# Kernel optimization log

Hardware: AMD Instinct MI355X
Metric: run time of the kernel (lower is better)

Reference implementation:

```python
import jax, jax.numpy as jnp
import numpy as np

N_NODES = 50000


def gcn_conv(x, src, dst, W, b):
    # PyG GCNConv: h = x @ W; symmetric norm with added self-loops; out = A_hat h + b
    h = x @ W
    deg = jax.ops.segment_sum(jnp.ones_like(src, dtype=h.dtype), dst,
                              num_segments=N_NODES) + 1.0  # +1 self-loop
    dis = jax.lax.rsqrt(deg)  # deg >= 1, safe
    msg = h[src] * (dis[src] * dis[dst])[:, None]          # [E,H] gather + scale
    agg = jax.ops.segment_sum(msg, dst, num_segments=N_NODES)
    agg = agg + h * (dis * dis)[:, None]                   # self-loop contribution
    return agg + b


def link_pred(zs, e, Wp, bp):
    # zs: [L,N,H]; gather endpoints along node dim, per-edge cross-layer Gram matrix
    s = zs[:, e[0]]                                # [L,E,H]
    d = zs[:, e[1]]                                # [L,E,H]
    dot = jnp.einsum('leh,meh->elm', s, d)         # [E,L,L] per-edge bmm
    emb = dot.reshape(dot.shape[0], -1)            # [E,L*L]
    return emb @ Wp + bp                           # [E,1] logits (activation=False)


def reference(x, ei, pos, neg, W0, b0, Wh, bh, Wp, bp):
    src, dst = ei[0], ei[1]
    h = jax.nn.relu(gcn_conv(x, src, dst, W0, b0))
    embs = [h]
    for i in range(Wh.shape[0]):  # fixed small layer count
        h = jax.nn.relu(gcn_conv(h, src, dst, Wh[i], bh[i]))
        embs.append(h)
    zs = jnp.stack(embs, axis=0)                   # [L,N,H]
    pos_pred = link_pred(zs, pos, Wp, bp)
    neg_pred = link_pred(zs, neg, Wp, bp)
    logits = jnp.concatenate([pos_pred, neg_pred], axis=0)  # [2E,1]
    # faithful to source: targets all zero except row index == n_pos set to 1
    targets = jnp.zeros_like(logits).at[pos_pred.shape[0]].set(1.0)
    # BCEWithLogitsLoss (mean, numerically stable)
    loss = jnp.mean(jnp.clip(logits, 0.0) - logits * targets
                    + jnp.log1p(jnp.exp(-jnp.abs(logits))))
    return loss


def setup_inputs():
    key = jax.random.key(0)
    ks = jax.random.split(key, 10)
    N, E, EP, IN, H, L = 50000, 800000, 100000, 128, 64, 4
    x = jax.random.normal(ks[0], (N, IN), jnp.float32)
    ei = jax.random.randint(ks[1], (2, E), 0, N, dtype=jnp.int32)
    pos = jax.random.randint(ks[2], (2, EP), 0, N, dtype=jnp.int32)
    neg = jax.random.randint(ks[3], (2, EP), 0, N, dtype=jnp.int32)
    def u(k, shape, fan_in):
        s = 1.0 / np.sqrt(fan_in)
        return jax.random.uniform(k, shape, jnp.float32, -s, s)
    W0 = u(ks[4], (IN, H), IN)
    b0 = u(ks[5], (H,), IN)
    Wh = u(ks[6], (L - 1, H, H), H)
    bh = u(ks[7], (L - 1, H), H)
    Wp = u(ks[8], (L * L, 1), L * L)
    bp = u(ks[9], (1,), L * L)
    return {"x": x, "ei": ei, "pos": pos, "neg": neg, "W0": W0, "b0": b0,
            "Wh": Wh, "bh": bh, "Wp": Wp, "bp": bp}
```

## Files before the change

kernel.cpp:

```cpp
#include <hip/hip_runtime.h>
#include <hip/hip_bf16.h>
#include <math.h>

constexpr int N_NODES = 50000;
constexpr int HD = 64;
constexpr int NBKT = (N_NODES + 255) / 256;

typedef float floatx2 __attribute__((ext_vector_type(2)));

__device__ __forceinline__ float bf2f(unsigned short u) {
    return __uint_as_float((unsigned)u << 16);
}
__device__ __forceinline__ unsigned short f2bf(float f) {
    __hip_bfloat16 b = __float2bfloat16(f);
    return *(unsigned short*)&b;
}
__device__ __forceinline__ unsigned pack_fp8x4(float a, float b, float c, float d) {
    unsigned p = __builtin_amdgcn_cvt_pk_fp8_f32(a, b, 0u, false);
    return __builtin_amdgcn_cvt_pk_fp8_f32(c, d, p, true);
}
__device__ __forceinline__ float dot16_fp8(uint4 u, uint4 d) {
    const unsigned uu[4] = {u.x, u.y, u.z, u.w};
    const unsigned dd[4] = {d.x, d.y, d.z, d.w};
    float s = 0.f;
#pragma unroll
    for (int q = 0; q < 4; ++q) {
        floatx2 ua = __builtin_amdgcn_cvt_pk_f32_fp8(uu[q], false);
        floatx2 ub = __builtin_amdgcn_cvt_pk_f32_fp8(uu[q], true);
        floatx2 da = __builtin_amdgcn_cvt_pk_f32_fp8(dd[q], false);
        floatx2 db = __builtin_amdgcn_cvt_pk_f32_fp8(dd[q], true);
        s = fmaf(ua[0], da[0], s);
        s = fmaf(ua[1], da[1], s);
        s = fmaf(ub[0], db[0], s);
        s = fmaf(ub[1], db[1], s);
    }
    return s;
}

__global__ __launch_bounds__(256) void bhist_kernel(const int* __restrict__ dst,
                                                    int* __restrict__ bcnt, int E) {
    __shared__ int lh[256];
    const int t = threadIdx.x;
    lh[t] = 0;
    __syncthreads();
    const int beg = blockIdx.x * 2048;
    const int end = min(beg + 2048, E);
    for (int i = beg + t; i < end; i += 256)
        atomicAdd(&lh[dst[i] >> 8], 1);
    __syncthreads();
    if (t < NBKT && lh[t]) atomicAdd(&bcnt[t], lh[t]);
}

__global__ __launch_bounds__(256) void bscan_kernel(const int* __restrict__ bcnt,
                                                    int* __restrict__ bbase,
                                                    int* __restrict__ gcur) {
    const int t = threadIdx.x;
    const int v = (t < NBKT) ? bcnt[t] : 0;
    const int lane = t & 63, wid = t >> 6;
    int incl = v;
#pragma unroll
    for (int o = 1; o <= 32; o <<= 1) {
        int u = __shfl_up(incl, o);
        if (lane >= o) incl += u;
    }
    __shared__ int wt[4];
    if (lane == 63) wt[wid] = incl;
    __syncthreads();
    int base = 0;
    for (int w = 0; w < wid; ++w) base += wt[w];
    const int excl = base + incl - v;
    if (t < NBKT) { bbase[t] = excl; gcur[t] = excl; }
    if (t == NBKT - 1) bbase[NBKT] = excl + v;
}

__global__ __launch_bounds__(256) void partition_kernel(const int* __restrict__ src,
                                                        const int* __restrict__ dst,
                                                        int* __restrict__ gcur,
                                                        unsigned* __restrict__ pk, int E) {
    __shared__ unsigned epk[8192];
    __shared__ int lh[NBKT], lbase[NBKT], lcur[NBKT];
    const int t = threadIdx.x;
    for (int i = t; i < NBKT; i += 256) { lh[i] = 0; lcur[i] = 0; }
    __syncthreads();
    const int beg = blockIdx.x * 8192;
    const int end = min(beg + 8192, E);
    for (int i = beg + t; i < end; i += 256) {
        const int s = src[i], d = dst[i];
        const int bkt = d >> 8;
        epk[i - beg] = ((unsigned)bkt << 24) | ((unsigned)(d & 255) << 16) | (unsigned)s;
        atomicAdd(&lh[bkt], 1);
    }
    __syncthreads();
    for (int i = t; i < NBKT; i += 256)
        if (lh[i]) lbase[i] = atomicAdd(&gcur[i], lh[i]);
    __syncthreads();
    for (int i = beg + t; i < end; i += 256) {
        const unsigned p = epk[i - beg];
        const int bkt = p >> 24;
        const int r = atomicAdd(&lcur[bkt], 1);
        pk[lbase[bkt] + r] = p;
    }
}

__global__ __launch_bounds__(256) void bsort_kernel(const unsigned* __restrict__ pk,
                                                    const int* __restrict__ bbase,
                                                    int* __restrict__ off,
                                                    float* __restrict__ dis,
                                                    int* __restrict__ csr, int E, int N) {
    __shared__ int ncnt[256], nbs[256], ncur[256];
    __shared__ int wt[4];
    const int t = threadIdx.x;
    const int bkt = blockIdx.x;
    const int gb = bbase[bkt], ge = bbase[bkt + 1];
    ncnt[t] = 0; ncur[t] = 0;
    __syncthreads();
    for (int i = gb + t; i < ge; i += 256)
        atomicAdd(&ncnt[(pk[i] >> 16) & 255], 1);
    __syncthreads();
    const int v = ncnt[t];
    const int lane = t & 63, wid = t >> 6;
    int incl = v;
#pragma unroll
    for (int o = 1; o <= 32; o <<= 1) {
        int u = __shfl_up(incl, o);
        if (lane >= o) incl += u;
    }
    if (lane == 63) wt[wid] = incl;
    __syncthreads();
    int base = 0;
    for (int w = 0; w < wid; ++w) base += wt[w];
    nbs[t] = base + incl - v;
    const int n = bkt * 256 + t;
    if (n < N) {
        off[n] = gb + nbs[t];
        dis[n] = rsqrtf((float)v + 1.0f);
        if (n == N - 1) off[N] = E;
    }
    __syncthreads();
    for (int i = gb + t; i < ge; i += 256) {
        const unsigned p = pk[i];
        const int dl = (p >> 16) & 255;
        const int r = atomicAdd(&ncur[dl], 1);
        csr[gb + nbs[dl] + r] = (int)(p & 0xFFFFu);
    }
}

template <int K, bool INBF16>
__global__ __launch_bounds__(256) void gemm_kernel(const void* __restrict__ in_,
                                                   const float* __restrict__ W,
                                                   unsigned short* __restrict__ out16,
                                                   unsigned* __restrict__ out8, int N) {
    __shared__ float xs[64][68];
    __shared__ float Wl[64][64];
    const int t = threadIdx.x;
    const int row0 = blockIdx.x * 64;
    const int cq = t & 15, rq = t >> 4;
    float acc[4][4] = {{0.f}};
    for (int kc = 0; kc < K; kc += 64) {
#pragma unroll
        for (int it = 0; it < 4; ++it) {
            const int idx = it * 256 + t;
            const int r = idx >> 4, c4 = idx & 15;
            const int rr = min(row0 + r, N - 1);
            if constexpr (INBF16) {
                const unsigned short* in16 = (const unsigned short*)in_;
                const ushort4 v = *(const ushort4*)(in16 + (size_t)rr * K + kc + c4 * 4);
                *(float4*)(&xs[r][c4 * 4]) = make_float4(bf2f(v.x), bf2f(v.y), bf2f(v.z), bf2f(v.w));
            } else {
                const float* inf = (const float*)in_;
                *(float4*)(&xs[r][c4 * 4]) = *(const float4*)(inf + (size_t)rr * K + kc + c4 * 4);
            }
            *(float4*)(&Wl[r][c4 * 4]) = *(const float4*)(W + (size_t)(kc + r) * HD + c4 * 4);
        }
        __syncthreads();
#pragma unroll
        for (int k4 = 0; k4 < 16; ++k4) {
            float a[4][4], b[4][4];
#pragma unroll
            for (int i = 0; i < 4; ++i)
                *(float4*)a[i] = *(const float4*)(&xs[rq * 4 + i][k4 * 4]);
#pragma unroll
            for (int kk = 0; kk < 4; ++kk)
                *(float4*)b[kk] = *(const float4*)(&Wl[k4 * 4 + kk][cq * 4]);
#pragma unroll
            for (int kk = 0; kk < 4; ++kk)
#pragma unroll
                for (int i = 0; i < 4; ++i)
#pragma unroll
                    for (int j = 0; j < 4; ++j)
                        acc[i][j] = fmaf(a[i][kk], b[kk][j], acc[i][j]);
        }
        __syncthreads();
    }
#pragma unroll
    for (int i = 0; i < 4; ++i) {
        const int r = row0 + rq * 4 + i;
        if (r < N) {
            ushort4 o;
            o.x = f2bf(acc[i][0]); o.y = f2bf(acc[i][1]);
            o.z = f2bf(acc[i][2]); o.w = f2bf(acc[i][3]);
            *(ushort4*)(out16 + (size_t)r * HD + cq * 4) = o;
            out8[(size_t)r * 16 + cq] = pack_fp8x4(acc[i][0], acc[i][1], acc[i][2], acc[i][3]);
        }
    }
}

__global__ __launch_bounds__(256) void agg_kernel(const int* __restrict__ csr,
                                                  const int* __restrict__ off,
                                                  const float* __restrict__ dis,
                                                  const unsigned short* __restrict__ h16,
                                                  const unsigned* __restrict__ h8,
                                                  const float* __restrict__ b,
                                                  unsigned short* __restrict__ z16, int N) {
    const int lane = threadIdx.x & 63;
    const int wid  = threadIdx.x >> 6;
    const int n = blockIdx.x * 4 + wid;
    if (n >= N) return;
    const int beg = off[n];
    const int c = min(off[n + 1] - beg, 64);
    int   s_l = 0;
    float w_l = 0.f;
    if (lane < c) {
        s_l = csr[beg + lane];
        w_l = dis[s_l];
    }
    const float dn = dis[n];
    const int g = lane >> 3;
    const int p = lane & 7;
    float a[8];
#pragma unroll
    for (int j = 0; j < 8; ++j) a[j] = 0.f;
    int   sE = __shfl(s_l, g);
    float wE = __shfl(w_l, g);
    uint2 hv = *(const uint2*)(h8 + (size_t)sE * 16 + p * 2);
    for (int e = 8; e < c; e += 8) {
        const int   sN = __shfl(s_l, e + g);
        const float wN = __shfl(w_l, e + g);
        const uint2 nv = *(const uint2*)(h8 + (size_t)sN * 16 + p * 2);
        floatx2 f01 = __builtin_amdgcn_cvt_pk_f32_fp8(hv.x, false);
        floatx2 f23 = __builtin_amdgcn_cvt_pk_f32_fp8(hv.x, true);
        floatx2 f45 = __builtin_amdgcn_cvt_pk_f32_fp8(hv.y, false);
        floatx2 f67 = __builtin_amdgcn_cvt_pk_f32_fp8(hv.y, true);
        a[0] = fmaf(f01[0], wE, a[0]); a[1] = fmaf(f01[1], wE, a[1]);
        a[2] = fmaf(f23[0], wE, a[2]); a[3] = fmaf(f23[1], wE, a[3]);
        a[4] = fmaf(f45[0], wE, a[4]); a[5] = fmaf(f45[1], wE, a[5]);
        a[6] = fmaf(f67[0], wE, a[6]); a[7] = fmaf(f67[1], wE, a[7]);
        hv = nv; wE = wN;
    }
    {
        floatx2 f01 = __builtin_amdgcn_cvt_pk_f32_fp8(hv.x, false);
        floatx2 f23 = __builtin_amdgcn_cvt_pk_f32_fp8(hv.x, true);
        floatx2 f45 = __builtin_amdgcn_cvt_pk_f32_fp8(hv.y, false);
        floatx2 f67 = __builtin_amdgcn_cvt_pk_f32_fp8(hv.y, true);
        a[0] = fmaf(f01[0], wE, a[0]); a[1] = fmaf(f01[1], wE, a[1]);
        a[2] = fmaf(f23[0], wE, a[2]); a[3] = fmaf(f23[1], wE, a[3]);
        a[4] = fmaf(f45[0], wE, a[4]); a[5] = fmaf(f45[1], wE, a[5]);
        a[6] = fmaf(f67[0], wE, a[6]); a[7] = fmaf(f67[1], wE, a[7]);
    }
#pragma unroll
    for (int st = 8; st <= 32; st <<= 1)
#pragma unroll
        for (int j = 0; j < 8; ++j) a[j] += __shfl_xor(a[j], st);
    if (g == 0) {
        const uint4 sv = *(const uint4*)(h16 + (size_t)n * HD + p * 8);
        const unsigned ss[4] = {sv.x, sv.y, sv.z, sv.w};
        const float4 b0 = *(const float4*)(b + p * 8);
        const float4 b1 = *(const float4*)(b + p * 8 + 4);
        const float bb[8] = {b0.x, b0.y, b0.z, b0.w, b1.x, b1.y, b1.z, b1.w};
        float o[8];
#pragma unroll
        for (int q = 0; q < 4; ++q) {
            o[2 * q]     = a[2 * q]     + __uint_as_float(ss[q] << 16) * dn;
            o[2 * q + 1] = a[2 * q + 1] + __uint_as_float(ss[q] & 0xFFFF0000u) * dn;
        }
#pragma unroll
        for (int j = 0; j < 8; ++j) o[j] = fmaxf(fmaf(o[j], dn, bb[j]), 0.f);
        ushort4 o0, o1;
        o0.x = f2bf(o[0]); o0.y = f2bf(o[1]); o0.z = f2bf(o[2]); o0.w = f2bf(o[3]);
        o1.x = f2bf(o[4]); o1.y = f2bf(o[5]); o1.z = f2bf(o[6]); o1.w = f2bf(o[7]);
        unsigned short* zp = z16 + (size_t)n * HD + p * 8;
        *(ushort4*)zp = o0;
        *(ushort4*)(zp + 4) = o1;
    }
}

__global__ __launch_bounds__(256) void uprep_kernel(const unsigned short* __restrict__ z16,
                                                    const float* __restrict__ Wp,
                                                    unsigned* __restrict__ u8,
                                                    unsigned* __restrict__ d8, int N) {
    const int i = blockIdx.x * blockDim.x + threadIdx.x;
    const int total = N * HD;
    if (i >= total) return;
    const size_t NH = (size_t)N_NODES * HD;
    const float z0 = bf2f(z16[0 * NH + i]), z1 = bf2f(z16[1 * NH + i]);
    const float z2 = bf2f(z16[2 * NH + i]), z3 = bf2f(z16[3 * NH + i]);
    d8[i] = pack_fp8x4(z0, z1, z2, z3);
    const float u0 = z0 * Wp[0] + z1 * Wp[4] + z2 * Wp[8]  + z3 * Wp[12];
    const float u1 = z0 * Wp[1] + z1 * Wp[5] + z2 * Wp[9]  + z3 * Wp[13];
    const float u2 = z0 * Wp[2] + z1 * Wp[6] + z2 * Wp[10] + z3 * Wp[14];
    const float u3 = z0 * Wp[3] + z1 * Wp[7] + z2 * Wp[11] + z3 * Wp[15];
    u8[i] = pack_fp8x4(u0, u1, u2, u3);
}

__global__ __launch_bounds__(256) void linkpred_kernel(const unsigned* __restrict__ u8,
                                                       const unsigned* __restrict__ d8,
                                                       const int* __restrict__ pos,
                                                       const int* __restrict__ neg,
                                                       const float* __restrict__ bp,
                                                       double* __restrict__ acc, int EP) {
    const int lane = threadIdx.x & 63;
    const int wid  = threadIdx.x >> 6;
    const int grp  = lane >> 4;
    const int p    = lane & 15;
    const float bpv = bp[0];
    int gw = blockIdx.x * 4 + wid;
    const int nw = gridDim.x * 4;
    const int nchunks = (2 * EP) >> 3;
    float lsum = 0.f;
    for (int c0 = gw; c0 < nchunks; c0 += nw) {
        const int c = __builtin_amdgcn_readfirstlane(c0);
        const int i0 = c << 3;
        const bool is_pos = i0 < EP;
        const int* __restrict__ eptr = is_pos ? pos : neg;
        const int jj0 = is_pos ? i0 : i0 - EP;
        int idx = 0;
        if (lane < 16)
            idx = (lane < 8) ? eptr[jj0 + lane] : eptr[EP + jj0 + lane - 8];
        const int e0a = __shfl(idx, grp),     e1a = __shfl(idx, 8 + grp);
        const int e0b = __shfl(idx, 4 + grp), e1b = __shfl(idx, 12 + grp);
        const uint4 ua = *(const uint4*)(u8 + (size_t)e0a * HD + p * 4);
        const uint4 da = *(const uint4*)(d8 + (size_t)e1a * HD + p * 4);
        const uint4 ub = *(const uint4*)(u8 + (size_t)e0b * HD + p * 4);
        const uint4 db = *(const uint4*)(d8 + (size_t)e1b * HD + p * 4);
        float tA = dot16_fp8(ua, da);
        float tB = dot16_fp8(ub, db);
#pragma unroll
        for (int st = 1; st <= 8; st <<= 1) {
            tA += __shfl_xor(tA, st);
            tB += __shfl_xor(tB, st);
        }
        const float ga = __shfl(tA, (lane & 3) * 16);
        const float gb = __shfl(tB, (lane & 3) * 16);
        const float tt = (lane < 4) ? ga : gb;
        if (lane < 8) {
            float logit  = tt + bpv;
            float target = (i0 + lane == EP) ? 1.f : 0.f;
            lsum += fmaxf(logit, 0.f) - logit * target + log1pf(expf(-fabsf(logit)));
        }
    }
#pragma unroll
    for (int o = 32; o >= 1; o >>= 1) lsum += __shfl_xor(lsum, o);
    __shared__ float wsum[4];
    if (lane == 0) wsum[wid] = lsum;
    __syncthreads();
    if (threadIdx.x == 0) {
        double bs = (double)wsum[0] + (double)wsum[1] + (double)wsum[2] + (double)wsum[3];
        atomicAdd(acc, bs);
    }
}

__global__ void loss_final(const double* __restrict__ acc, float* __restrict__ out, int denom) {
    out[0] = (float)(acc[0] / (double)denom);
}

extern "C" void kernel_launch(void* const* d_in, const int* in_sizes, int n_in,
                              void* d_out, int out_size, void* d_ws, size_t ws_size,
                              hipStream_t stream) {
    const float* x   = (const float*)d_in[0];
    const int*   ei  = (const int*)d_in[1];
    const int*   pos = (const int*)d_in[2];
    const int*   neg = (const int*)d_in[3];
    const float* W0  = (const float*)d_in[4];
    const float* b0  = (const float*)d_in[5];
    const float* Wh  = (const float*)d_in[6];
    const float* bh  = (const float*)d_in[7];
    const float* Wp  = (const float*)d_in[8];
    const float* bp  = (const float*)d_in[9];
    const int E  = in_sizes[1] / 2;
    const int EP = in_sizes[2] / 2;
    const int N  = N_NODES;
    const size_t NH = (size_t)N * HD;

    char* ws = (char*)d_ws;
    size_t off_b = 0;
    auto alloc = [&](size_t bytes) { char* p = ws + off_b; off_b = (off_b + bytes + 255) & ~(size_t)255; return p; };
    unsigned short* h16 = (unsigned short*)alloc(NH * sizeof(unsigned short));
    unsigned*       h8  = (unsigned*)alloc(NH);
    unsigned short* z16 = (unsigned short*)alloc(4 * NH * sizeof(unsigned short));
    unsigned*       u8  = (unsigned*)alloc(NH * sizeof(unsigned));
    unsigned*       d8  = (unsigned*)alloc(NH * sizeof(unsigned));
    float* dis = (float*)alloc((size_t)N * sizeof(float));
    int*   off = (int*)alloc((size_t)(N + 1) * sizeof(int));
    int*   csr = (int*)alloc((size_t)E * sizeof(int));
    unsigned* pk = (unsigned*)alloc((size_t)E * sizeof(unsigned));
    int*   bbase = (int*)alloc((size_t)(NBKT + 1) * sizeof(int));
    int*   gcur  = (int*)alloc((size_t)NBKT * sizeof(int));
    char*  zbase = ws + off_b;
    int*   bcnt = (int*)alloc((size_t)NBKT * sizeof(int));
    double* acc = (double*)alloc(sizeof(double));
    size_t zero_bytes = (size_t)((char*)acc - zbase) + sizeof(double);

    hipMemsetAsync(zbase, 0, zero_bytes, stream);

    const int* src = ei;
    const int* dst = ei + E;

    bhist_kernel<<<(E + 2047) / 2048, 256, 0, stream>>>(dst, bcnt, E);
    bscan_kernel<<<1, 256, 0, stream>>>(bcnt, bbase, gcur);
    partition_kernel<<<(E + 8191) / 8192, 256, 0, stream>>>(src, dst, gcur, pk, E);
    bsort_kernel<<<NBKT, 256, 0, stream>>>(pk, bbase, off, dis, csr, E, N);

    const int agg_blocks  = (N + 3) / 4;
    const int gemm_blocks = (N + 63) / 64;

    gemm_kernel<128, false><<<gemm_blocks, 256, 0, stream>>>(x, W0, h16, h8, N);
    agg_kernel<<<agg_blocks, 256, 0, stream>>>(csr, off, dis, h16, h8, b0, z16, N);

    for (int l = 1; l < 4; ++l) {
        unsigned short* zprev = z16 + (size_t)(l - 1) * NH;
        unsigned short* zcur  = z16 + (size_t)l * NH;
        gemm_kernel<64, true><<<gemm_blocks, 256, 0, stream>>>(zprev, Wh + (size_t)(l - 1) * HD * HD, h16, h8, N);
        agg_kernel<<<agg_blocks, 256, 0, stream>>>(csr, off, dis, h16, h8,
                                                   bh + (size_t)(l - 1) * HD, zcur, N);
    }

    uprep_kernel<<<(N * HD + 255) / 256, 256, 0, stream>>>(z16, Wp, u8, d8, N);
    linkpred_kernel<<<2048, 256, 0, stream>>>(u8, d8, pos, neg, bp, acc, EP);
    loss_final<<<1, 1, 0, stream>>>(acc, (float*)d_out, 2 * EP);
}
```

Baseline: 276.7 us.

## Fuse first GEMM with histogram, uprep into final aggregation, loss finalize into linkpred

Folds the degree-bucket histogram into the first GEMM launch as extra blocks, so the two independent jobs share one grid. The separate uprep pass moves into the last aggregation kernel, which builds the fp8 u/d tensors from the fresh layer output and the earlier layers it already has in hand. The final loss division moves into linkpred through an atomic ticket on the last block. The goal is fewer kernel launches and one fewer full pass over z16, at the cost of a heavier final aggregation kernel and a ticket-based completion check.

```diff
diff --git a/kernel.cpp b/kernel.cpp
--- a/kernel.cpp
+++ b/kernel.cpp
@@ -37,18 +37,70 @@
     return s;
 }
 
-__global__ __launch_bounds__(256) void bhist_kernel(const int* __restrict__ dst,
-                                                    int* __restrict__ bcnt, int E) {
-    __shared__ int lh[256];
+__global__ __launch_bounds__(256) void gemm128_bhist_kernel(
+        const float* __restrict__ in_, const float* __restrict__ W,
+        unsigned short* __restrict__ out16, unsigned* __restrict__ out8,
+        const int* __restrict__ dst, int* __restrict__ bcnt,
+        int N, int E, int nGemm) {
+    __shared__ float xs[64][68];
+    __shared__ float Wl[64][64];
     const int t = threadIdx.x;
-    lh[t] = 0;
-    __syncthreads();
-    const int beg = blockIdx.x * 2048;
-    const int end = min(beg + 2048, E);
-    for (int i = beg + t; i < end; i += 256)
-        atomicAdd(&lh[dst[i] >> 8], 1);
-    __syncthreads();
-    if (t < NBKT && lh[t]) atomicAdd(&bcnt[t], lh[t]);
+    if ((int)blockIdx.x >= nGemm) {
+        int* lh = (int*)&xs[0][0];
+        lh[t] = 0;
+        __syncthreads();
+        const int beg = ((int)blockIdx.x - nGemm) * 2048;
+        const int end = min(beg + 2048, E);
+        for (int i = beg + t; i < end; i += 256)
+            atomicAdd(&lh[dst[i] >> 8], 1);
+        __syncthreads();
+        if (t < NBKT && lh[t]) atomicAdd(&bcnt[t], lh[t]);
+        return;
+    }
+    constexpr int K = 128;
+    const int row0 = blockIdx.x * 64;
+    const int cq = t & 15, rq = t >> 4;
+    float acc[4][4] = {{0.f}};
+    for (int kc = 0; kc < K; kc += 64) {
+#pragma unroll
+        for (int it = 0; it < 4; ++it) {
+            const int idx = it * 256 + t;
+            const int r = idx >> 4, c4 = idx & 15;
+            const int rr = min(row0 + r, N - 1);
+            *(float4*)(&xs[r][c4 * 4]) = *(const float4*)(in_ + (size_t)rr * K + kc + c4 * 4);
+            *(float4*)(&Wl[r][c4 * 4]) = *(const float4*)(W + (size_t)(kc + r) * HD + c4 * 4);
+        }
+        __syncthreads();
+#pragma unroll
+        for (int k4 = 0; k4 < 16; ++k4) {
+            float a[4][4], b[4][4];
+#pragma unroll
+            for (int i = 0; i < 4; ++i)
+                *(float4*)a[i] = *(const float4*)(&xs[rq * 4 + i][k4 * 4]);
+#pragma unroll
+            for (int kk = 0; kk < 4; ++kk)
+                *(float4*)b[kk] = *(const float4*)(&Wl[k4 * 4 + kk][cq * 4]);
+#pragma unroll
+            for (int kk = 0; kk < 4; ++kk)
+#pragma unroll
+                for (int i = 0; i < 4; ++i)
+#pragma unroll
+                    for (int j = 0; j < 4; ++j)
+                        acc[i][j] = fmaf(a[i][kk], b[kk][j], acc[i][j]);
+        }
+        __syncthreads();
+    }
+#pragma unroll
+    for (int i = 0; i < 4; ++i) {
+        const int r = row0 + rq * 4 + i;
+        if (r < N) {
+            ushort4 o;
+            o.x = f2bf(acc[i][0]); o.y = f2bf(acc[i][1]);
+            o.z = f2bf(acc[i][2]); o.w = f2bf(acc[i][3]);
+            *(ushort4*)(out16 + (size_t)r * HD + cq * 4) = o;
+            out8[(size_t)r * 16 + cq] = pack_fp8x4(acc[i][0], acc[i][1], acc[i][2], acc[i][3]);
+        }
+    }
 }
 
 __global__ __launch_bounds__(256) void bscan_kernel(const int* __restrict__ bcnt,
@@ -145,32 +197,26 @@
     }
 }
 
-template <int K, bool INBF16>
-__global__ __launch_bounds__(256) void gemm_kernel(const void* __restrict__ in_,
-                                                   const float* __restrict__ W,
-                                                   unsigned short* __restrict__ out16,
-                                                   unsigned* __restrict__ out8, int N) {
+__global__ __launch_bounds__(256) void gemm64_kernel(const unsigned short* __restrict__ in16,
+                                                     const float* __restrict__ W,
+                                                     unsigned short* __restrict__ out16,
+                                                     unsigned* __restrict__ out8, int N) {
+    constexpr int K = 64;
     __shared__ float xs[64][68];
     __shared__ float Wl[64][64];
     const int t = threadIdx.x;
     const int row0 = blockIdx.x * 64;
     const int cq = t & 15, rq = t >> 4;
     float acc[4][4] = {{0.f}};
-    for (int kc = 0; kc < K; kc += 64) {
+    {
 #pragma unroll
         for (int it = 0; it < 4; ++it) {
             const int idx = it * 256 + t;
             const int r = idx >> 4, c4 = idx & 15;
             const int rr = min(row0 + r, N - 1);
-            if constexpr (INBF16) {
-                const unsigned short* in16 = (const unsigned short*)in_;
-                const ushort4 v = *(const ushort4*)(in16 + (size_t)rr * K + kc + c4 * 4);
-                *(float4*)(&xs[r][c4 * 4]) = make_float4(bf2f(v.x), bf2f(v.y), bf2f(v.z), bf2f(v.w));
-            } else {
-                const float* inf = (const float*)in_;
-                *(float4*)(&xs[r][c4 * 4]) = *(const float4*)(inf + (size_t)rr * K + kc + c4 * 4);
-            }
-            *(float4*)(&Wl[r][c4 * 4]) = *(const float4*)(W + (size_t)(kc + r) * HD + c4 * 4);
+            const ushort4 v = *(const ushort4*)(in16 + (size_t)rr * K + c4 * 4);
+            *(float4*)(&xs[r][c4 * 4]) = make_float4(bf2f(v.x), bf2f(v.y), bf2f(v.z), bf2f(v.w));
+            *(float4*)(&Wl[r][c4 * 4]) = *(const float4*)(W + (size_t)r * HD + c4 * 4);
         }
         __syncthreads();
 #pragma unroll
@@ -190,7 +236,6 @@
                     for (int j = 0; j < 4; ++j)
                         acc[i][j] = fmaf(a[i][kk], b[kk][j], acc[i][j]);
         }
-        __syncthreads();
     }
 #pragma unroll
     for (int i = 0; i < 4; ++i) {
@@ -205,13 +250,18 @@
     }
 }
 
+template <bool FINAL>
 __global__ __launch_bounds__(256) void agg_kernel(const int* __restrict__ csr,
                                                   const int* __restrict__ off,
                                                   const float* __restrict__ dis,
                                                   const unsigned short* __restrict__ h16,
                                                   const unsigned* __restrict__ h8,
                                                   const float* __restrict__ b,
-                                                  unsigned short* __restrict__ z16, int N) {
+                                                  unsigned short* __restrict__ z16out,
+                                                  const unsigned short* __restrict__ zall,
+                                                  const float* __restrict__ Wp,
+                                                  unsigned* __restrict__ u8,
+                                                  unsigned* __restrict__ d8, int N) {
     const int lane = threadIdx.x & 63;
     const int wid  = threadIdx.x >> 6;
     const int n = blockIdx.x * 4 + wid;
@@ -273,33 +323,45 @@
             o[2 * q]     = a[2 * q]     + __uint_as_float(ss[q] << 16) * dn;
             o[2 * q + 1] = a[2 * q + 1] + __uint_as_float(ss[q] & 0xFFFF0000u) * dn;
         }
-#pragma unroll
-        for (int j = 0; j < 8; ++j) o[j] = fmaxf(fmaf(o[j], dn, bb[j]), 0.f);
-        ushort4 o0, o1;
-        o0.x = f2bf(o[0]); o0.y = f2bf(o[1]); o0.z = f2bf(o[2]); o0.w = f2bf(o[3]);
-        o1.x = f2bf(o[4]); o1.y = f2bf(o[5]); o1.z = f2bf(o[6]); o1.w = f2bf(o[7]);
-        unsigned short* zp = z16 + (size_t)n * HD + p * 8;
-        *(ushort4*)zp = o0;
-        *(ushort4*)(zp + 4) = o1;
-    }
-}
-
-__global__ __launch_bounds__(256) void uprep_kernel(const unsigned short* __restrict__ z16,
-                                                    const float* __restrict__ Wp,
-                                                    unsigned* __restrict__ u8,
-                                                    unsigned* __restrict__ d8, int N) {
-    const int i = blockIdx.x * blockDim.x + threadIdx.x;
-    const int total = N * HD;
-    if (i >= total) return;
-    const size_t NH = (size_t)N_NODES * HD;
-    const float z0 = bf2f(z16[0 * NH + i]), z1 = bf2f(z16[1 * NH + i]);
-    const float z2 = bf2f(z16[2 * NH + i]), z3 = bf2f(z16[3 * NH + i]);
-    d8[i] = pack_fp8x4(z0, z1, z2, z3);
-    const float u0 = z0 * Wp[0] + z1 * Wp[4] + z2 * Wp[8]  + z3 * Wp[12];
-    const float u1 = z0 * Wp[1] + z1 * Wp[5] + z2 * Wp[9]  + z3 * Wp[13];
-    const float u2 = z0 * Wp[2] + z1 * Wp[6] + z2 * Wp[10] + z3 * Wp[14];
-    const float u3 = z0 * Wp[3] + z1 * Wp[7] + z2 * Wp[11] + z3 * Wp[15];
-    u8[i] = pack_fp8x4(u0, u1, u2, u3);
+        unsigned short z3b[8];
+#pragma unroll
+        for (int j = 0; j < 8; ++j) {
+            const float v = fmaxf(fmaf(o[j], dn, bb[j]), 0.f);
+            z3b[j] = f2bf(v);
+        }
+        unsigned short* zp = z16out + (size_t)n * HD + p * 8;
+        *(ushort4*)zp = *(ushort4*)z3b;
+        *(ushort4*)(zp + 4) = *(ushort4*)(z3b + 4);
+        if constexpr (FINAL) {
+            const size_t NH = (size_t)N_NODES * HD;
+            const unsigned short* l0 = zall + 0 * NH + (size_t)n * HD + p * 8;
+            const unsigned short* l1 = zall + 1 * NH + (size_t)n * HD + p * 8;
+            const unsigned short* l2 = zall + 2 * NH + (size_t)n * HD + p * 8;
+            unsigned short L0[8], L1[8], L2[8];
+            *(ushort4*)L0 = *(const ushort4*)l0; *(ushort4*)(L0 + 4) = *(const ushort4*)(l0 + 4);
+            *(ushort4*)L1 = *(const ushort4*)l1; *(ushort4*)(L1 + 4) = *(const ushort4*)(l1 + 4);
+            *(ushort4*)L2 = *(const ushort4*)l2; *(ushort4*)(L2 + 4) = *(const ushort4*)(l2 + 4);
+            float wpc[16];
+#pragma unroll
+            for (int m = 0; m < 16; ++m) wpc[m] = Wp[m];
+            unsigned uo[8], dvo[8];
+#pragma unroll
+            for (int j = 0; j < 8; ++j) {
+                const float v0 = bf2f(L0[j]), v1 = bf2f(L1[j]);
+                const float v2 = bf2f(L2[j]), v3 = bf2f(z3b[j]);
+                dvo[j] = pack_fp8x4(v0, v1, v2, v3);
+                const float u0v = v0 * wpc[0] + v1 * wpc[4] + v2 * wpc[8]  + v3 * wpc[12];
+                const float u1v = v0 * wpc[1] + v1 * wpc[5] + v2 * wpc[9]  + v3 * wpc[13];
+                const float u2v = v0 * wpc[2] + v1 * wpc[6] + v2 * wpc[10] + v3 * wpc[14];
+                const float u3v = v0 * wpc[3] + v1 * wpc[7] + v2 * wpc[11] + v3 * wpc[15];
+                uo[j] = pack_fp8x4(u0v, u1v, u2v, u3v);
+            }
+            unsigned* up = u8 + (size_t)n * HD + p * 8;
+            unsigned* dp = d8 + (size_t)n * HD + p * 8;
+            *(uint4*)up = *(uint4*)uo;  *(uint4*)(up + 4) = *(uint4*)(uo + 4);
+            *(uint4*)dp = *(uint4*)dvo; *(uint4*)(dp + 4) = *(uint4*)(dvo + 4);
+        }
+    }
 }
 
 __global__ __launch_bounds__(256) void linkpred_kernel(const unsigned* __restrict__ u8,
@@ -307,7 +369,9 @@
                                                        const int* __restrict__ pos,
                                                        const int* __restrict__ neg,
                                                        const float* __restrict__ bp,
-                                                       double* __restrict__ acc, int EP) {
+                                                       double* __restrict__ acc,
+                                                       unsigned* __restrict__ ticket,
+                                                       float* __restrict__ outp, int EP) {
     const int lane = threadIdx.x & 63;
     const int wid  = threadIdx.x >> 6;
     const int grp  = lane >> 4;
@@ -356,11 +420,14 @@
     if (threadIdx.x == 0) {
         double bs = (double)wsum[0] + (double)wsum[1] + (double)wsum[2] + (double)wsum[3];
         atomicAdd(acc, bs);
-    }
-}
-
-__global__ void loss_final(const double* __restrict__ acc, float* __restrict__ out, int denom) {
-    out[0] = (float)(acc[0] / (double)denom);
+        __threadfence();
+        const unsigned done = atomicAdd(ticket, 1u);
+        if (done == gridDim.x - 1) {
+            __threadfence();
+            const double v = *((volatile double*)acc);
+            outp[0] = (float)(v / (double)(2 * EP));
+        }
+    }
 }
 
 extern "C" void kernel_launch(void* const* d_in, const int* in_sizes, int n_in,
@@ -397,6 +464,7 @@
     int*   gcur  = (int*)alloc((size_t)NBKT * sizeof(int));
     char*  zbase = ws + off_b;
     int*   bcnt = (int*)alloc((size_t)NBKT * sizeof(int));
+    unsigned* ticket = (unsigned*)alloc(sizeof(unsigned));
     double* acc = (double*)alloc(sizeof(double));
     size_t zero_bytes = (size_t)((char*)acc - zbase) + sizeof(double);
 
@@ -405,26 +473,34 @@
     const int* src = ei;
     const int* dst = ei + E;
 
-    bhist_kernel<<<(E + 2047) / 2048, 256, 0, stream>>>(dst, bcnt, E);
+    const int gemm_blocks = (N + 63) / 64;
+    const int bhist_blocks = (E + 2047) / 2048;
+    const int agg_blocks  = (N + 3) / 4;
+
+    gemm128_bhist_kernel<<<gemm_blocks + bhist_blocks, 256, 0, stream>>>(
+        x, W0, h16, h8, dst, bcnt, N, E, gemm_blocks);
     bscan_kernel<<<1, 256, 0, stream>>>(bcnt, bbase, gcur);
     partition_kernel<<<(E + 8191) / 8192, 256, 0, stream>>>(src, dst, gcur, pk, E);
     bsort_kernel<<<NBKT, 256, 0, stream>>>(pk, bbase, off, dis, csr, E, N);
 
-    const int agg_blocks  = (N + 3) / 4;
-    const int gemm_blocks = (N + 63) / 64;
-
-    gemm_kernel<128, false><<<gemm_blocks, 256, 0, stream>>>(x, W0, h16, h8, N);
-    agg_kernel<<<agg_blocks, 256, 0, stream>>>(csr, off, dis, h16, h8, b0, z16, N);
+    agg_kernel<false><<<agg_blocks, 256, 0, stream>>>(csr, off, dis, h16, h8, b0,
+                                                      z16, z16, Wp, u8, d8, N);
 
     for (int l = 1; l < 4; ++l) {
         unsigned short* zprev = z16 + (size_t)(l - 1) * NH;
         unsigned short* zcur  = z16 + (size_t)l * NH;
-        gemm_kernel<64, true><<<gemm_blocks, 256, 0, stream>>>(zprev, Wh + (size_t)(l - 1) * HD * HD, h16, h8, N);
-        agg_kernel<<<agg_blocks, 256, 0, stream>>>(csr, off, dis, h16, h8,
-                                                   bh + (size_t)(l - 1) * HD, zcur, N);
-    }
-
-    uprep_kernel<<<(N * HD + 255) / 256, 256, 0, stream>>>(z16, Wp, u8, d8, N);
-    linkpred_kernel<<<2048, 256, 0, stream>>>(u8, d8, pos, neg, bp, acc, EP);
-    loss_final<<<1, 1, 0, stream>>>(acc, (float*)d_out, 2 * EP);
-}
+        gemm64_kernel<<<gemm_blocks, 256, 0, stream>>>(zprev, Wh + (size_t)(l - 1) * HD * HD, h16, h8, N);
+        if (l < 3) {
+            agg_kernel<false><<<agg_blocks, 256, 0, stream>>>(csr, off, dis, h16, h8,
+                                                              bh + (size_t)(l - 1) * HD,
+                                                              zcur, z16, Wp, u8, d8, N);
+        } else {
+            agg_kernel<true><<<agg_blocks, 256, 0, stream>>>(csr, off, dis, h16, h8,
+                                                             bh + (size_t)(l - 1) * HD,
+                                                             zcur, z16, Wp, u8, d8, N);
+        }
+    }
+
+    linkpred_kernel<<<2048, 256, 0, stream>>>(u8, d8, pos, neg, bp, acc, ticket,
+                                              (float*)d_out, EP);
+}
```

Result: slower. 309.1 us (+11.7%).
